# Kernel optimization log

Hardware: AMD Instinct MI355X
Metric: run time of the kernel (lower is better)

## Reference

```python
import jax, jax.numpy as jnp
import numpy as np

# __init__ defaults of BoxSelector
NMS_T = 0.5
TOP_K = 400
CONF_T = 0.5
KEEP_K = 200
# standard SSD BoxCoder variances
V0, V1 = 0.1, 0.2
BIG = 1e9
B, N, C = 128, 32768, 6  # batch, num_priors, 4 loc + 2 classes


def decode(loc, priors):
    # SSD decode: priors are (cx, cy, w, h); returns (x1, y1, x2, y2)
    cxcy = priors[:, :2] + loc[:, :2] * V0 * priors[:, 2:]
    wh = priors[:, 2:] * jnp.exp(loc[:, 2:] * V1)
    return jnp.concatenate([cxcy - wh * 0.5, cxcy + wh * 0.5], axis=1)


def pairwise_iou(b):
    # b: [K, 4] xyxy -> [K, K] IoU
    x1, y1, x2, y2 = b[:, 0], b[:, 1], b[:, 2], b[:, 3]
    area = (x2 - x1) * (y2 - y1)
    iw = jnp.clip(jnp.minimum(x2[:, None], x2[None, :]) - jnp.maximum(x1[:, None], x1[None, :]), 0.0)
    ih = jnp.clip(jnp.minimum(y2[:, None], y2[None, :]) - jnp.maximum(y1[:, None], y1[None, :]), 0.0)
    inter = iw * ih
    return inter / (area[:, None] + area[None, :] - inter + 1e-12)


def _select_image(pred, priorboxes):
    loc, confs = pred[:, :4], pred[:, 4:]
    boxes = decode(loc, priorboxes)                       # [N, 4]
    scores = jnp.max(confs, axis=1)                       # [N]
    labels = jnp.argmax(confs, axis=1)                    # [N] int
    # confidence filter (mask instead of dynamic gather, jit-friendly)
    masked = jnp.where(scores > CONF_T, scores, -BIG)
    top_s, idx = jax.lax.top_k(masked, TOP_K)             # descending, [K]
    cand_boxes = boxes[idx]                               # [K, 4]
    cand_labels = labels[idx]                             # [K]
    valid = top_s > CONF_T                                # padding from filter
    # greedy NMS over the top_k candidates (already score-sorted desc)
    iou = pairwise_iou(cand_boxes)                        # [K, K]
    j = jnp.arange(TOP_K)
    def body(i, keep):
        sup = keep[i] & (iou[i] > NMS_T) & (j > i)
        return keep & ~sup
    keep = jax.lax.fori_loop(0, TOP_K, body, valid)
    # original sorts kept scores ASCENDING and takes the first keep_top_k
    sort_key = jnp.where(keep, top_s, BIG)                # invalid sort last
    order = jnp.argsort(sort_key)[:KEEP_K]                # [keep_top_k]
    out = jnp.concatenate(
        [cand_labels[order, None].astype(jnp.float32),
         top_s[order, None],
         cand_boxes[order]], axis=1)                      # [keep_top_k, 6]
    return jnp.where(keep[order][:, None], out, 0.0)


def setup_inputs() -> dict:
    key = jax.random.key(0)
    k1, k2 = jax.random.split(key)
    predictions = jax.random.normal(k1, (B, N, C), dtype=jnp.float32)
    priors = jax.random.uniform(k2, (N, 4), dtype=jnp.float32)
    return {"predictions": predictions, "priors": priors}


def reference(predictions, priors):
    priorboxes = priors[:, :4]
    return jax.vmap(lambda p: _select_image(p, priorboxes))(predictions)  # [B, keep_top_k, 6]
```

## Files before the change

### kernel.cpp

```cpp
#include <hip/hip_runtime.h>
#include <stdint.h>

#define BB 128
#define NN 32768
#define CI 6
#define TOPK 400
#define KEEPK 200
#define SORTN 1024
#define NT 1024
#define KQT 8
#define NBUCK 4096
#define KEY0 0x3F000000u

#define IOU_C 0.50000002980232238769531250

__global__ __launch_bounds__(256) void score_kernel(
        const float* __restrict__ pred, uint32_t* __restrict__ keys) {
    int g = blockIdx.x * 256 + threadIdx.x;
    const float4* p4 = reinterpret_cast<const float4*>(pred) + (size_t)g * 3;
    float4 a = p4[0];
    float4 b = p4[1];
    float4 c = p4[2];
    asm volatile("" :: "v"(a.x));
    float s0 = fmaxf(b.x, b.y);
    float s1 = fmaxf(c.z, c.w);
    uint2 o;
    o.x = (s0 > 0.5f) ? __float_as_uint(s0) : 0u;
    o.y = (s1 > 0.5f) ? __float_as_uint(s1) : 0u;
    *reinterpret_cast<uint2*>(keys + (size_t)g * 2) = o;
}

__global__ __launch_bounds__(NT) void boxsel2_kernel(
        const float* __restrict__ pred, const float* __restrict__ priors,
        const uint32_t* __restrict__ keys, float* __restrict__ out) {
    const int b = blockIdx.x;
    const int tid = threadIdx.x;
    const int lane = tid & 63;
    const int wid = tid >> 6;
    const float* img = pred + (size_t)b * (NN * CI);
    float* oimg = out + (size_t)b * KEEPK * 6;

    __shared__ union {
        unsigned int hist[2][NBUCK];
        struct {
            unsigned long long cbuf[SORTN];
            unsigned long long cbuf2[SORTN];
            float4 cbox[TOPK];
            float car[TOPK], csc[TOPK];
            int clab[TOPK];
            unsigned long long supm[TOPK * 7 + 8];
        } s;
    } u;
    __shared__ unsigned int wavetot[16];
    __shared__ unsigned int sh_bucket, ccount;
    __shared__ unsigned long long keepw[8];

    for (int i = tid; i < KEEPK * 6; i += NT) oimg[i] = 0.0f;

    uint4 kq[KQT];
    const uint4* k4 = reinterpret_cast<const uint4*>(keys + (size_t)b * NN);
#pragma unroll
    for (int uu = 0; uu < KQT; uu++) kq[uu] = k4[tid + (uu << 10)];

    if (tid == 0) { sh_bucket = 0; ccount = 0; }
    if (tid < 8) keepw[tid] = 0ull;
    for (int i = tid; i < 2 * NBUCK; i += NT) ((unsigned int*)u.hist)[i] = 0u;
    __syncthreads();

    const int hc = wid & 1;
#pragma unroll
    for (int uu = 0; uu < KQT; uu++) {
        uint32_t k0 = kq[uu].x, k1 = kq[uu].y, k2 = kq[uu].z, k3 = kq[uu].w;
        if (k0) { unsigned int bu = (k0 - KEY0) >> 13; if (bu > NBUCK - 1u) bu = NBUCK - 1u; atomicAdd(&u.hist[hc][bu], 1u); }
        if (k1) { unsigned int bu = (k1 - KEY0) >> 13; if (bu > NBUCK - 1u) bu = NBUCK - 1u; atomicAdd(&u.hist[hc][bu], 1u); }
        if (k2) { unsigned int bu = (k2 - KEY0) >> 13; if (bu > NBUCK - 1u) bu = NBUCK - 1u; atomicAdd(&u.hist[hc][bu], 1u); }
        if (k3) { unsigned int bu = (k3 - KEY0) >> 13; if (bu > NBUCK - 1u) bu = NBUCK - 1u; atomicAdd(&u.hist[hc][bu], 1u); }
    }
    __syncthreads();

    unsigned int h0 = u.hist[0][4 * tid + 0] + u.hist[1][4 * tid + 0];
    unsigned int h1 = u.hist[0][4 * tid + 1] + u.hist[1][4 * tid + 1];
    unsigned int h2 = u.hist[0][4 * tid + 2] + u.hist[1][4 * tid + 2];
    unsigned int h3 = u.hist[0][4 * tid + 3] + u.hist[1][4 * tid + 3];
    unsigned int sum = h0 + h1 + h2 + h3;
    unsigned int suf = sum;
#pragma unroll
    for (int off = 1; off < 64; off <<= 1) {
        unsigned int v = __shfl_down(suf, off);
        if (lane + off < 64) suf += v;
    }
    if (lane == 0) wavetot[wid] = suf;
    __syncthreads();
    if (tid < 16) {
        unsigned int wv = wavetot[tid];
        unsigned int ws = wv;
#pragma unroll
        for (int off = 1; off < 16; off <<= 1) {
            unsigned int v = __shfl_down(ws, off);
            if (tid + off < 16) ws += v;
        }
        wavetot[tid] = ws - wv;
    }
    __syncthreads();
    unsigned int acc = wavetot[wid] + (suf - sum);
    if (acc < TOPK && acc + h3 >= TOPK) sh_bucket = 4 * tid + 3;
    acc += h3;
    if (acc < TOPK && acc + h2 >= TOPK) sh_bucket = 4 * tid + 2;
    acc += h2;
    if (acc < TOPK && acc + h1 >= TOPK) sh_bucket = 4 * tid + 1;
    acc += h1;
    if (acc < TOPK && acc + h0 >= TOPK) sh_bucket = 4 * tid + 0;
    __syncthreads();
    const uint32_t Tkey = KEY0 + (sh_bucket << 13);

    u.s.cbuf2[tid] = 0ull;
    __syncthreads();
#pragma unroll
    for (int uu = 0; uu < KQT; uu++) {
        uint32_t kk[4] = { kq[uu].x, kq[uu].y, kq[uu].z, kq[uu].w };
#pragma unroll
        for (int j = 0; j < 4; j++) {
            uint32_t key = kk[j];
            if (key >= Tkey) {
                unsigned int p = atomicAdd(&ccount, 1u);
                if (p < SORTN) {
                    unsigned int idx = ((unsigned int)(tid + (uu << 10)) << 2) + (unsigned int)j;
                    u.s.cbuf[p] = ((unsigned long long)key << 32) |
                                  (unsigned long long)(0xFFFFFFFFu - idx);
                }
            }
        }
    }
    __syncthreads();

    {
        const unsigned int cnt = (ccount < SORTN) ? ccount : SORTN;
        if ((unsigned int)tid < cnt) {
            unsigned long long ct = u.s.cbuf[tid];
            unsigned int rank = 0;
#pragma unroll 4
            for (unsigned int j = 0; j < cnt; j++)
                rank += (u.s.cbuf[j] > ct) ? 1u : 0u;
            u.s.cbuf2[rank] = ct;
        }
    }
    __syncthreads();

    for (int i2 = tid; i2 < TOPK * 7 + 8; i2 += NT) u.s.supm[i2] = 0ull;
    if (tid < TOPK) {
        const int t = tid;
        unsigned long long c = u.s.cbuf2[t];
        uint32_t key = (uint32_t)(c >> 32);
        uint32_t idx = 0xFFFFFFFFu - (uint32_t)(c & 0xFFFFFFFFull);
        int valid = (key != 0u) && (idx < NN);
        float x1 = 0.f, y1 = 0.f, x2 = 0.f, y2 = 0.f;
        int lab = 0;
        if (valid) {
            const float* p = img + (size_t)idx * CI;
            float l0 = p[0], l1 = p[1], l2 = p[2], l3 = p[3], c0 = p[4], c1 = p[5];
            const float* pr = priors + (size_t)idx * 4;
            float px = pr[0], py = pr[1], pw = pr[2], ph = pr[3];
            float cxv = __fadd_rn(px, __fmul_rn(__fmul_rn(l0, 0.1f), pw));
            float cyv = __fadd_rn(py, __fmul_rn(__fmul_rn(l1, 0.1f), ph));
            float ew = __fmul_rn(pw, expf(__fmul_rn(l2, 0.2f)));
            float eh = __fmul_rn(ph, expf(__fmul_rn(l3, 0.2f)));
            float hw = __fmul_rn(ew, 0.5f);
            float hh = __fmul_rn(eh, 0.5f);
            x1 = __fsub_rn(cxv, hw); y1 = __fsub_rn(cyv, hh);
            x2 = __fadd_rn(cxv, hw); y2 = __fadd_rn(cyv, hh);
            lab = (c1 > c0) ? 1 : 0;
        }
        u.s.cbox[t] = make_float4(x1, y1, x2, y2);
        u.s.csc[t] = __uint_as_float(key);
        u.s.car[t] = __fmul_rn(__fsub_rn(x2, x1), __fsub_rn(y2, y1));
        u.s.clab[t] = lab;
        if (valid) atomicOr(&keepw[t >> 6], 1ull << (t & 63));
    }
    __syncthreads();

    {
        float4 bjv[7]; float ajv[7];
#pragma unroll
        for (int jw = 0; jw < 7; jw++) {
            int j = (jw << 6) + lane;
            int jc = (j < TOPK) ? j : (TOPK - 1);
            bjv[jw] = u.s.cbox[jc];
            ajv[jw] = u.s.car[jc];
        }
        for (int i = wid; i < TOPK; i += 16) {
            float4 bi = u.s.cbox[i];
            float ai = u.s.car[i];
            const int jw0 = i >> 6;
#pragma unroll
            for (int jw = 0; jw < 7; jw++) {
                if (jw < jw0) continue;
                int j = (jw << 6) + lane;
                float4 bj = bjv[jw]; float aj = ajv[jw];
                float iw = fmaxf(__fsub_rn(fminf(bi.z, bj.z), fmaxf(bi.x, bj.x)), 0.0f);
                float ih = fmaxf(__fsub_rn(fminf(bi.w, bj.w), fmaxf(bi.y, bj.y)), 0.0f);
                float inter = __fmul_rn(iw, ih);
                float denom = __fadd_rn(__fsub_rn(__fadd_rn(ai, aj), inter), 1e-12f);
                bool bit = (j > i) && (j < TOPK) &&
                           ((double)inter > (double)denom * IOU_C);
                unsigned long long word = __ballot(bit);
                if (lane == 0) u.s.supm[i * 7 + jw] = word;
            }
        }
    }
    __syncthreads();

    if (tid < 64) {
        int w = tid & 7;
        unsigned long long kw = keepw[w];
        unsigned long long rr[16], nn[16];
#pragma unroll
        for (int k = 0; k < 16; k++) rr[k] = u.s.supm[k * 7 + w];
        for (int base = 0; base < TOPK; base += 16) {
            int nb = base + 16;
            int gb = (nb < TOPK) ? nb : base;
#pragma unroll
            for (int k = 0; k < 16; k++) nn[k] = u.s.supm[(gb + k) * 7 + w];
#pragma unroll
            for (int k = 0; k < 16; k++) {
                int i = base + k;
                unsigned long long wv = __shfl(kw, i >> 6);
                if ((wv >> (i & 63)) & 1ull) kw &= ~rr[k];
            }
#pragma unroll
            for (int k = 0; k < 16; k++) rr[k] = nn[k];
        }
        if (tid < 7) keepw[tid] = kw;
    }
    __syncthreads();

    if (tid < TOPK) {
        const int t = tid;
        if ((keepw[t >> 6] >> (t & 63)) & 1ull) {
            float st = u.s.csc[t];
            int rank = 0;
#pragma unroll
            for (int w = 0; w < 7; w++) {
                unsigned long long kws = keepw[w];
                int jb = w << 6;
                unsigned long long m;
                if (t >= jb + 63)      m = 0ull;
                else if (t < jb)       m = ~0ull;
                else                   m = ~((1ull << (t - jb + 1)) - 1ull);
                rank += __popcll(kws & m);
            }
            for (int j = t + 1; j < TOPK && u.s.csc[j] == st; j++)
                if ((keepw[j >> 6] >> (j & 63)) & 1ull) rank--;
            for (int j = t - 1; j >= 0 && u.s.csc[j] == st; j--)
                if ((keepw[j >> 6] >> (j & 63)) & 1ull) rank++;
            if (rank < KEEPK) {
                float4 bx = u.s.cbox[t];
                float* row = oimg + (size_t)rank * 6;
                row[0] = (float)u.s.clab[t];
                row[1] = st;
                row[2] = bx.x; row[3] = bx.y; row[4] = bx.z; row[5] = bx.w;
            }
        }
    }
}

extern "C" void kernel_launch(void* const* d_in, const int* in_sizes, int n_in,
                              void* d_out, int out_size, void* d_ws, size_t ws_size,
                              hipStream_t stream) {
    const float* pred = (const float*)d_in[0];
    const float* priors = (const float*)d_in[1];
    float* out = (float*)d_out;
    uint32_t* keys = (uint32_t*)d_ws;
    score_kernel<<<(BB * NN / 2) / 256, 256, 0, stream>>>(pred, keys);
    boxsel2_kernel<<<BB, NT, 0, stream>>>(pred, priors, keys, out);
}
```

Measured before the change: 204.9 us.

## Stage score tiles through LDS, fuse rank-sort with decode, widen histogram privatization

The score kernel now has each block load a 1024-prior tile into shared memory with coalesced float4 reads, and each thread emits four keys as a uint4. In the select kernel the separate rank-sort scatter buffer is removed: each candidate computes its rank and decodes its box in the same pass, writing directly to its sorted slot. The keep mask comes from the candidate count instead of atomics. The histogram gets four per-wave copies to reduce atomic contention, and the NMS shuffle becomes scalar readlanes. The cost is more LDS for the histogram and the score tile, and every candidate, not only the top 400, now decodes.

```diff
diff --git a/kernel.cpp b/kernel.cpp
--- a/kernel.cpp
+++ b/kernel.cpp
@@ -11,23 +11,26 @@
 #define KQT 8
 #define NBUCK 4096
 #define KEY0 0x3F000000u
+#define STILE 1024
 
 #define IOU_C 0.50000002980232238769531250
 
 __global__ __launch_bounds__(256) void score_kernel(
         const float* __restrict__ pred, uint32_t* __restrict__ keys) {
-    int g = blockIdx.x * 256 + threadIdx.x;
-    const float4* p4 = reinterpret_cast<const float4*>(pred) + (size_t)g * 3;
-    float4 a = p4[0];
-    float4 b = p4[1];
-    float4 c = p4[2];
-    asm volatile("" :: "v"(a.x));
-    float s0 = fmaxf(b.x, b.y);
-    float s1 = fmaxf(c.z, c.w);
-    uint2 o;
-    o.x = (s0 > 0.5f) ? __float_as_uint(s0) : 0u;
-    o.y = (s1 > 0.5f) ? __float_as_uint(s1) : 0u;
-    *reinterpret_cast<uint2*>(keys + (size_t)g * 2) = o;
+    __shared__ float lf[STILE * 6];
+    const int t = threadIdx.x;
+    const float4* p4 = reinterpret_cast<const float4*>(pred) +
+                       (size_t)blockIdx.x * (STILE * 6 / 4);
+    float4* l4 = reinterpret_cast<float4*>(lf);
+#pragma unroll
+    for (int k = 0; k < 6; k++) l4[t + 256 * k] = p4[t + 256 * k];
+    __syncthreads();
+    uint4 o;
+    { float s = fmaxf(lf[24 * t +  4], lf[24 * t +  5]); o.x = (s > 0.5f) ? __float_as_uint(s) : 0u; }
+    { float s = fmaxf(lf[24 * t + 10], lf[24 * t + 11]); o.y = (s > 0.5f) ? __float_as_uint(s) : 0u; }
+    { float s = fmaxf(lf[24 * t + 16], lf[24 * t + 17]); o.z = (s > 0.5f) ? __float_as_uint(s) : 0u; }
+    { float s = fmaxf(lf[24 * t + 22], lf[24 * t + 23]); o.w = (s > 0.5f) ? __float_as_uint(s) : 0u; }
+    reinterpret_cast<uint4*>(keys)[blockIdx.x * 256 + t] = o;
 }
 
 __global__ __launch_bounds__(NT) void boxsel2_kernel(
@@ -41,10 +44,9 @@
     float* oimg = out + (size_t)b * KEEPK * 6;
 
     __shared__ union {
-        unsigned int hist[2][NBUCK];
+        unsigned int hist[4][NBUCK];
         struct {
             unsigned long long cbuf[SORTN];
-            unsigned long long cbuf2[SORTN];
             float4 cbox[TOPK];
             float car[TOPK], csc[TOPK];
             int clab[TOPK];
@@ -63,11 +65,10 @@
     for (int uu = 0; uu < KQT; uu++) kq[uu] = k4[tid + (uu << 10)];
 
     if (tid == 0) { sh_bucket = 0; ccount = 0; }
-    if (tid < 8) keepw[tid] = 0ull;
-    for (int i = tid; i < 2 * NBUCK; i += NT) ((unsigned int*)u.hist)[i] = 0u;
-    __syncthreads();
-
-    const int hc = wid & 1;
+    for (int i = tid; i < 4 * NBUCK; i += NT) ((unsigned int*)u.hist)[i] = 0u;
+    __syncthreads();
+
+    const int hc = wid & 3;
 #pragma unroll
     for (int uu = 0; uu < KQT; uu++) {
         uint32_t k0 = kq[uu].x, k1 = kq[uu].y, k2 = kq[uu].z, k3 = kq[uu].w;
@@ -78,10 +79,10 @@
     }
     __syncthreads();
 
-    unsigned int h0 = u.hist[0][4 * tid + 0] + u.hist[1][4 * tid + 0];
-    unsigned int h1 = u.hist[0][4 * tid + 1] + u.hist[1][4 * tid + 1];
-    unsigned int h2 = u.hist[0][4 * tid + 2] + u.hist[1][4 * tid + 2];
-    unsigned int h3 = u.hist[0][4 * tid + 3] + u.hist[1][4 * tid + 3];
+    unsigned int h0 = u.hist[0][4 * tid + 0] + u.hist[1][4 * tid + 0] + u.hist[2][4 * tid + 0] + u.hist[3][4 * tid + 0];
+    unsigned int h1 = u.hist[0][4 * tid + 1] + u.hist[1][4 * tid + 1] + u.hist[2][4 * tid + 1] + u.hist[3][4 * tid + 1];
+    unsigned int h2 = u.hist[0][4 * tid + 2] + u.hist[1][4 * tid + 2] + u.hist[2][4 * tid + 2] + u.hist[3][4 * tid + 2];
+    unsigned int h3 = u.hist[0][4 * tid + 3] + u.hist[1][4 * tid + 3] + u.hist[2][4 * tid + 3] + u.hist[3][4 * tid + 3];
     unsigned int sum = h0 + h1 + h2 + h3;
     unsigned int suf = sum;
 #pragma unroll
@@ -113,8 +114,6 @@
     __syncthreads();
     const uint32_t Tkey = KEY0 + (sh_bucket << 13);
 
-    u.s.cbuf2[tid] = 0ull;
-    __syncthreads();
 #pragma unroll
     for (int uu = 0; uu < KQT; uu++) {
         uint32_t kk[4] = { kq[uu].x, kq[uu].y, kq[uu].z, kq[uu].w };
@@ -133,48 +132,39 @@
     }
     __syncthreads();
 
-    {
-        const unsigned int cnt = (ccount < SORTN) ? ccount : SORTN;
-        if ((unsigned int)tid < cnt) {
-            unsigned long long ct = u.s.cbuf[tid];
-            unsigned int rank = 0;
+    const unsigned int cnt = (ccount < SORTN) ? ccount : SORTN;
+    for (int i2 = tid; i2 < TOPK * 7 + 8; i2 += NT) u.s.supm[i2] = 0ull;
+    if (tid < 8) {
+        int cntc = (cnt < TOPK) ? (int)cnt : TOPK;
+        int rem = cntc - (tid << 6);
+        keepw[tid] = (rem <= 0) ? 0ull : ((rem >= 64) ? ~0ull : ((1ull << rem) - 1ull));
+    }
+    if ((unsigned int)tid < cnt) {
+        unsigned long long ct = u.s.cbuf[tid];
+        uint32_t key = (uint32_t)(ct >> 32);
+        uint32_t idx = 0xFFFFFFFFu - (uint32_t)(ct & 0xFFFFFFFFull);
+        const float* p = img + (size_t)idx * CI;
+        float l0 = p[0], l1 = p[1], l2 = p[2], l3 = p[3], c0 = p[4], c1 = p[5];
+        const float* pr = priors + (size_t)idx * 4;
+        float px = pr[0], py = pr[1], pw = pr[2], ph = pr[3];
+        unsigned int rank = 0;
 #pragma unroll 4
-            for (unsigned int j = 0; j < cnt; j++)
-                rank += (u.s.cbuf[j] > ct) ? 1u : 0u;
-            u.s.cbuf2[rank] = ct;
-        }
-    }
-    __syncthreads();
-
-    for (int i2 = tid; i2 < TOPK * 7 + 8; i2 += NT) u.s.supm[i2] = 0ull;
-    if (tid < TOPK) {
-        const int t = tid;
-        unsigned long long c = u.s.cbuf2[t];
-        uint32_t key = (uint32_t)(c >> 32);
-        uint32_t idx = 0xFFFFFFFFu - (uint32_t)(c & 0xFFFFFFFFull);
-        int valid = (key != 0u) && (idx < NN);
-        float x1 = 0.f, y1 = 0.f, x2 = 0.f, y2 = 0.f;
-        int lab = 0;
-        if (valid) {
-            const float* p = img + (size_t)idx * CI;
-            float l0 = p[0], l1 = p[1], l2 = p[2], l3 = p[3], c0 = p[4], c1 = p[5];
-            const float* pr = priors + (size_t)idx * 4;
-            float px = pr[0], py = pr[1], pw = pr[2], ph = pr[3];
-            float cxv = __fadd_rn(px, __fmul_rn(__fmul_rn(l0, 0.1f), pw));
-            float cyv = __fadd_rn(py, __fmul_rn(__fmul_rn(l1, 0.1f), ph));
-            float ew = __fmul_rn(pw, expf(__fmul_rn(l2, 0.2f)));
-            float eh = __fmul_rn(ph, expf(__fmul_rn(l3, 0.2f)));
-            float hw = __fmul_rn(ew, 0.5f);
-            float hh = __fmul_rn(eh, 0.5f);
-            x1 = __fsub_rn(cxv, hw); y1 = __fsub_rn(cyv, hh);
-            x2 = __fadd_rn(cxv, hw); y2 = __fadd_rn(cyv, hh);
-            lab = (c1 > c0) ? 1 : 0;
-        }
-        u.s.cbox[t] = make_float4(x1, y1, x2, y2);
-        u.s.csc[t] = __uint_as_float(key);
-        u.s.car[t] = __fmul_rn(__fsub_rn(x2, x1), __fsub_rn(y2, y1));
-        u.s.clab[t] = lab;
-        if (valid) atomicOr(&keepw[t >> 6], 1ull << (t & 63));
+        for (unsigned int j = 0; j < cnt; j++)
+            rank += (u.s.cbuf[j] > ct) ? 1u : 0u;
+        float cxv = __fadd_rn(px, __fmul_rn(__fmul_rn(l0, 0.1f), pw));
+        float cyv = __fadd_rn(py, __fmul_rn(__fmul_rn(l1, 0.1f), ph));
+        float ew = __fmul_rn(pw, expf(__fmul_rn(l2, 0.2f)));
+        float eh = __fmul_rn(ph, expf(__fmul_rn(l3, 0.2f)));
+        float hw = __fmul_rn(ew, 0.5f);
+        float hh = __fmul_rn(eh, 0.5f);
+        float x1 = __fsub_rn(cxv, hw), y1 = __fsub_rn(cyv, hh);
+        float x2 = __fadd_rn(cxv, hw), y2 = __fadd_rn(cyv, hh);
+        if (rank < TOPK) {
+            u.s.cbox[rank] = make_float4(x1, y1, x2, y2);
+            u.s.car[rank] = __fmul_rn(__fsub_rn(x2, x1), __fsub_rn(y2, y1));
+            u.s.csc[rank] = __uint_as_float(key);
+            u.s.clab[rank] = (c1 > c0) ? 1 : 0;
+        }
     }
     __syncthreads();
 
@@ -223,8 +213,10 @@
 #pragma unroll
             for (int k = 0; k < 16; k++) {
                 int i = base + k;
-                unsigned long long wv = __shfl(kw, i >> 6);
-                if ((wv >> (i & 63)) & 1ull) kw &= ~rr[k];
+                unsigned int lo = (unsigned int)__builtin_amdgcn_readlane((int)(unsigned int)kw, i >> 6);
+                unsigned int hi = (unsigned int)__builtin_amdgcn_readlane((int)(unsigned int)(kw >> 32), i >> 6);
+                unsigned int sel = ((i & 63) < 32) ? lo : hi;
+                if ((sel >> (i & 31)) & 1u) kw &= ~rr[k];
             }
 #pragma unroll
             for (int k = 0; k < 16; k++) rr[k] = nn[k];
@@ -270,6 +262,6 @@
     const float* priors = (const float*)d_in[1];
     float* out = (float*)d_out;
     uint32_t* keys = (uint32_t*)d_ws;
-    score_kernel<<<(BB * NN / 2) / 256, 256, 0, stream>>>(pred, keys);
+    score_kernel<<<(BB * NN) / STILE, 256, 0, stream>>>(pred, keys);
     boxsel2_kernel<<<BB, NT, 0, stream>>>(pred, priors, keys, out);
 }
```

After: 199.6 us. -2.6%, faster.
